# Kernel tuning notes

Measured on AMD Instinct MI355X. Metric: run time of the kernel, lower is better.

Reference implementation:

```python
import jax, jax.numpy as jnp
import numpy as np

N, D, E = 16384, 2048, 64   # tokens, d_model, num_experts
K = 9                        # self.k = min(k+1, num_experts) with k=8
EPS = 0.01
SIGMA = 1.0 / E              # Normal(0, 1/num_experts) stddev


def setup_inputs() -> dict:
    key = jax.random.key(0)
    ks = jax.random.split(key, 6)
    x = jax.random.normal(ks[0], (N, D), jnp.float32)
    Wr = jax.random.normal(ks[1], (D, E), jnp.float32) * 0.02
    br = jnp.zeros((E,), jnp.float32)
    Wn = jax.random.normal(ks[2], (D, E), jnp.float32) * 0.02
    bn = jnp.zeros((E,), jnp.float32)
    noise_eps = jax.random.normal(ks[3], (N, E), jnp.float32)
    # torch: (-empty.exponential_()).log() -> log of Exp(1) samples
    gumbel_noise = jnp.log(jax.random.exponential(ks[4], (N, E), jnp.float32))
    return {"x": x, "Wr": Wr, "br": br, "Wn": Wn, "bn": bn,
            "noise_eps": noise_eps, "gumbel_noise": gumbel_noise}


def reference(x, Wr, br, Wn, bn, noise_eps, gumbel_noise):
    raw_logits = x @ Wr + br                              # [N, E]
    noise_stddev = jax.nn.softplus(x @ Wn + bn) + EPS     # [N, E]
    noisy_logits = raw_logits + noise_eps * noise_stddev  # [N, E]

    top_vals, top_idx = jax.lax.top_k(noisy_logits, K)    # [N, K] sorted desc
    # scatter ones at top-k indices (indices unique per row)
    hard_mask = jax.nn.one_hot(top_idx, E, dtype=noisy_logits.dtype).sum(axis=1)  # [N, E]

    # gumbel-softmax straight-through relaxation
    mask_soft = jax.nn.softmax(noisy_logits + gumbel_noise, axis=-1)
    expert_mask = hard_mask - jax.lax.stop_gradient(mask_soft) + mask_soft

    route_prob = jax.nn.softmax(noisy_logits, axis=-1)    # [N, E]
    importance = jax.nn.softmax(raw_logits, axis=-1).sum(axis=0)  # [E]

    # load: P(raw + noise > threshold), Normal(0, 1/E) CDF per original
    threshold = top_vals[:, K - 1]                        # [N]
    z = (threshold[:, None] - raw_logits) / noise_stddev  # [N, E]
    cdf = 0.5 * (1.0 + jax.scipy.special.erf(z / (SIGMA * jnp.sqrt(jnp.float32(2.0)))))
    load = (1.0 - cdf).sum(axis=0)                        # [E]

    return (expert_mask, route_prob, importance, load)
```

## Files before the change

### kernel.cpp

```cpp
#include <hip/hip_runtime.h>
#include <hip/hip_bf16.h>
#include <math.h>

#define N_TOK 16384
#define DIM   2048
#define NE    64
#define TOPK  9

#define ROWS     32
#define DC       64
#define NCHUNK   (DIM / DC)
#define HALF     (NCHUNK / 2)
#define NTHREADS 512
#define NBUF     4

typedef short  short8  __attribute__((ext_vector_type(8)));
typedef float  float4_ __attribute__((ext_vector_type(4)));
typedef unsigned short ushort_t;

__device__ __forceinline__ void async16(const void* g, void* l) {
    __builtin_amdgcn_global_load_lds(
        (const __attribute__((address_space(1))) void*)g,
        (__attribute__((address_space(3))) void*)l, 16, 0, 0);
}

__device__ __forceinline__ unsigned pk2(float a, float b) {
    float2 f; f.x = a; f.y = b;
    __hip_bfloat162 h = __float22bfloat162_rn(f);
    unsigned u;
    __builtin_memcpy(&u, &h, 4);
    return u;
}

__device__ __forceinline__ void cvt8(const float4_ va, const float4_ vb,
                                     short8* h, short8* l) {
    union { short8 s; unsigned u[4]; } H, L;
    const float f[8] = {va[0], va[1], va[2], va[3], vb[0], vb[1], vb[2], vb[3]};
#pragma unroll
    for (int i = 0; i < 4; ++i) {
        const float a = f[2 * i], b = f[2 * i + 1];
        const unsigned p = pk2(a, b);
        H.u[i] = p;
        const float ha = __uint_as_float(p << 16);
        const float hb = __uint_as_float(p & 0xffff0000u);
        L.u[i] = pk2(a - ha, b - hb);
    }
    *h = H.s; *l = L.s;
}

__device__ __forceinline__ void wave_max64_2(float& a, float& b) {
#pragma unroll
    for (int off = 32; off > 0; off >>= 1) {
        const float ax = __shfl_xor(a, off, 64);
        const float bx = __shfl_xor(b, off, 64);
        a = fmaxf(a, ax);
        b = fmaxf(b, bx);
    }
}

__device__ __forceinline__ void wave_sum64_3(float& a, float& b, float& c) {
#pragma unroll
    for (int off = 32; off > 0; off >>= 1) {
        const float ax = __shfl_xor(a, off, 64);
        const float bx = __shfl_xor(b, off, 64);
        const float cx = __shfl_xor(c, off, 64);
        a += ax;
        b += bx;
        c += cx;
    }
}

__global__ __launch_bounds__(256)
void prep_w(const float* __restrict__ Wr, const float* __restrict__ Wn,
            ushort_t* __restrict__ wsW)
{
    const int gid = blockIdx.x * 256 + threadIdx.x;
    const int l   = gid & 63;
    const int ct  = (gid >> 6) & 7;
    const int kcg = gid >> 9;
    const int n   = ct * 16 + (l & 15);
    const int k0  = kcg * 32 + (l >> 4) * 8;
    const float* src = (n < NE) ? (Wr + n) : (Wn + (n - NE));
    union { short8 s; ushort_t us[8]; } H, L;
#pragma unroll
    for (int j = 0; j < 8; ++j) {
        const float v = src[(size_t)(k0 + j) * NE];
        const unsigned uv = __float_as_uint(v);
        const unsigned hb = (uv + 0x7fffu + ((uv >> 16) & 1u)) & 0xffff0000u;
        const float lo = v - __uint_as_float(hb);
        const unsigned ul = __float_as_uint(lo);
        H.us[j] = (ushort_t)(hb >> 16);
        L.us[j] = (ushort_t)((ul + 0x7fffu + ((ul >> 16) & 1u)) >> 16);
    }
    const size_t s0 = (size_t)(kcg * 8 + ct) * 2;
    *(short8*)(wsW + s0 * 512 + l * 8)         = H.s;
    *(short8*)(wsW + (s0 + 1) * 512 + l * 8)   = L.s;
}

struct BFrag { short8 h[2][2]; short8 l[2][2]; };

__device__ __forceinline__ void load_b(const char* __restrict__ wsB,
                                       int ch, int cg, int lane, BFrag& b) {
#pragma unroll
    for (int kc = 0; kc < 2; ++kc)
#pragma unroll
        for (int cc = 0; cc < 2; ++cc) {
            const size_t off = (size_t)(((ch * 2 + kc) * 8) + 2 * cg + cc) * 2048
                             + (size_t)lane * 16;
            b.h[kc][cc] = *(const short8*)(wsB + off);
            b.l[kc][cc] = *(const short8*)(wsB + off + 1024);
        }
}

__device__ __forceinline__ void mfma_chunk(const float* __restrict__ xb,
                                           const int (&aoff)[2][2],
                                           const BFrag& b,
                                           float4_ (&acc)[2][2]) {
#pragma unroll
    for (int kc = 0; kc < 2; ++kc)
#pragma unroll
        for (int rt = 0; rt < 2; ++rt) {
            const float4_ va = *(const float4_*)(xb + rt * 1024 + aoff[kc][0]);
            const float4_ vb = *(const float4_*)(xb + rt * 1024 + aoff[kc][1]);
            short8 ah, al;
            cvt8(va, vb, &ah, &al);
#pragma unroll
            for (int cc = 0; cc < 2; ++cc) {
                acc[rt][cc] = __builtin_amdgcn_mfma_f32_16x16x32_bf16(ah, b.h[kc][cc], acc[rt][cc], 0, 0, 0);
                acc[rt][cc] = __builtin_amdgcn_mfma_f32_16x16x32_bf16(al, b.h[kc][cc], acc[rt][cc], 0, 0, 0);
                acc[rt][cc] = __builtin_amdgcn_mfma_f32_16x16x32_bf16(ah, b.l[kc][cc], acc[rt][cc], 0, 0, 0);
            }
        }
}

__global__ __launch_bounds__(NTHREADS, 4)
void moe_main(const float* __restrict__ x,
              const float* __restrict__ br,
              const float* __restrict__ bn,
              const float* __restrict__ noise_eps,
              const float* __restrict__ gumbel,
              const ushort_t* __restrict__ wsW,
              float* __restrict__ out)
{
    __shared__ __align__(16) float smem[2 * NBUF * 2048];

    const int t    = threadIdx.x;
    const int lane = t & 63;
    const int w    = t >> 6;
    const int kh   = w >> 2;
    const int wv   = w & 3;
    const int c4   = lane & 15;
    const int q    = lane >> 4;
    const int row0 = blockIdx.x * ROWS;
    const int XB   = kh * (NBUF * 2048);

    const float* gxb[2];
    int lxo[2];
#pragma unroll
    for (int ii = 0; ii < 2; ++ii) {
        const int i  = 2 * wv + ii;
        const int r  = 4 * i + q;
        const int gk = c4 ^ (r & 15);
        gxb[ii] = x + (size_t)(row0 + r) * DIM + kh * (HALF * DC) + gk * 4;
        lxo[ii] = i * 256;
    }

    int aoff[2][2];
#pragma unroll
    for (int kc = 0; kc < 2; ++kc) {
        const int g0 = kc * 8 + q * 2;
        aoff[kc][0] = c4 * 64 + ((g0 ^ c4) * 4);
        aoff[kc][1] = c4 * 64 + (((g0 + 1) ^ c4) * 4);
    }

    float4_ acc[2][2];
#pragma unroll
    for (int rt = 0; rt < 2; ++rt)
#pragma unroll
        for (int cc = 0; cc < 2; ++cc)
            acc[rt][cc] = (float4_)(0.f);

    const char* wsB = (const char*)wsW;
    const int chb = kh * HALF;

#pragma unroll
    for (int p = 0; p < NBUF - 1; ++p)
#pragma unroll
        for (int ii = 0; ii < 2; ++ii)
            async16(gxb[ii] + p * DC, &smem[XB + p * 2048 + lxo[ii]]);

    BFrag bA, bB;
    load_b(wsB, chb, wv, lane, bA);

#pragma unroll 1
    for (int i = 0; i < HALF - 4; i += 2) {
        asm volatile("s_waitcnt vmcnt(12)" ::: "memory");
        __builtin_amdgcn_s_barrier();
        asm volatile("" ::: "memory");
        load_b(wsB, chb + i + 1, wv, lane, bB);
#pragma unroll
        for (int ii = 0; ii < 2; ++ii)
            async16(gxb[ii] + (i + 3) * DC, &smem[XB + ((i + 3) & 3) * 2048 + lxo[ii]]);
        __builtin_amdgcn_sched_barrier(0);
        mfma_chunk(&smem[XB + (i & 3) * 2048], aoff, bA, acc);

        asm volatile("s_waitcnt vmcnt(12)" ::: "memory");
        __builtin_amdgcn_s_barrier();
        asm volatile("" ::: "memory");
        load_b(wsB, chb + i + 2, wv, lane, bA);
#pragma unroll
        for (int ii = 0; ii < 2; ++ii)
            async16(gxb[ii] + (i + 4) * DC, &smem[XB + ((i + 4) & 3) * 2048 + lxo[ii]]);
        __builtin_amdgcn_sched_barrier(0);
        mfma_chunk(&smem[XB + ((i + 1) & 3) * 2048], aoff, bB, acc);
    }

    asm volatile("s_waitcnt vmcnt(12)" ::: "memory");
    __builtin_amdgcn_s_barrier();
    asm volatile("" ::: "memory");
    load_b(wsB, chb + 13, wv, lane, bB);
#pragma unroll
    for (int ii = 0; ii < 2; ++ii)
        async16(gxb[ii] + 15 * DC, &smem[XB + 3 * 2048 + lxo[ii]]);
    __builtin_amdgcn_sched_barrier(0);
    mfma_chunk(&smem[XB + 0 * 2048], aoff, bA, acc);

    asm volatile("s_waitcnt vmcnt(12)" ::: "memory");
    __builtin_amdgcn_s_barrier();
    asm volatile("" ::: "memory");
    load_b(wsB, chb + 14, wv, lane, bA);
    __builtin_amdgcn_sched_barrier(0);
    mfma_chunk(&smem[XB + 1 * 2048], aoff, bB, acc);

    asm volatile("s_waitcnt vmcnt(10)" ::: "memory");
    __builtin_amdgcn_s_barrier();
    asm volatile("" ::: "memory");
    load_b(wsB, chb + 15, wv, lane, bB);
    __builtin_amdgcn_sched_barrier(0);
    mfma_chunk(&smem[XB + 2 * 2048], aoff, bA, acc);

    asm volatile("s_waitcnt vmcnt(8)" ::: "memory");
    __builtin_amdgcn_s_barrier();
    asm volatile("" ::: "memory");
    __builtin_amdgcn_sched_barrier(0);
    mfma_chunk(&smem[XB + 3 * 2048], aoff, bB, acc);

    __syncthreads();
    {
        float* base = &smem[kh * 4160];
#pragma unroll
        for (int rt = 0; rt < 2; ++rt)
#pragma unroll
            for (int cc = 0; cc < 2; ++cc) {
                const int colg = (2 * wv + cc) * 16 + c4;
                float* bp = (colg < NE) ? base : (base + 2080);
                const int col = colg & 63;
#pragma unroll
                for (int v = 0; v < 4; ++v) {
                    const int row = rt * 16 + q * 4 + v;
                    bp[row * 65 + col] = acc[rt][cc][v];
                }
            }
    }
    __syncthreads();

    const float br_l = br[lane];
    const float bn_l = bn[lane];

    float epsv[4], gumv[4];
#pragma unroll
    for (int r = 0; r < 4; ++r) {
        const int row = row0 + w * 4 + r;
        epsv[r] = noise_eps[(size_t)row * NE + lane];
        gumv[r] = gumbel  [(size_t)row * NE + lane];
    }

    float imp_acc = 0.f, load_acc = 0.f;
    float* out_em   = out;
    float* out_rp   = out + (size_t)N_TOK * NE;
    float* out_imp  = out + (size_t)2 * N_TOK * NE;
    float* out_load = out_imp + NE;

#pragma unroll 1
    for (int r = 0; r < 4; ++r) {
        const int lrow = w * 4 + r;
        const int row  = row0 + lrow;
        const float raw = smem[lrow * 65 + lane] + smem[4160 + lrow * 65 + lane] + br_l;
        const float nl  = smem[2080 + lrow * 65 + lane] + smem[6240 + lrow * 65 + lane] + bn_l;
        const float sd = fmaxf(nl, 0.f) + log1pf(expf(-fabsf(nl))) + 0.01f;
        const float noisy = fmaf(epsv[r], sd, raw);

        const unsigned uk  = __float_as_uint(noisy);
        const unsigned key = uk ^ ((uk & 0x80000000u) ? 0xFFFFFFFFu : 0x80000000u);
        unsigned res = 0;
#pragma unroll
        for (int bit = 31; bit >= 0; --bit) {
            const unsigned cand = res | (1u << bit);
            const int cnt = __popcll(__ballot(key >= cand));
            if (cnt >= TOPK) res = cand;
        }
        const float thr  = __uint_as_float(res ^ ((res & 0x80000000u) ? 0x80000000u : 0xFFFFFFFFu));
        const float hard = (key >= res) ? 1.f : 0.f;

        const float g = noisy + gumv[r];
        float mg = g, mr = raw;
        wave_max64_2(mg, mr);

        const float eg = expf(g - mg);
        const float en = expf(noisy - thr);
        const float er = expf(raw - mr);
        float sg = eg, sn = en, sr = er;
        wave_sum64_3(sg, sn, sr);

        const float ms = eg / sg;
        const float em = (hard - ms) + ms;
        const float rp = en / sn;
        imp_acc += er / sr;

        const float z = (thr - raw) / sd;
        load_acc += 0.5f * erfcf(z * 45.254833995939045f);

        out_em[(size_t)row * NE + lane] = em;
        out_rp[(size_t)row * NE + lane] = rp;
    }

    __syncthreads();
    smem[w * 64 + lane]       = imp_acc;
    smem[512 + w * 64 + lane] = load_acc;
    __syncthreads();
    if (w == 0) {
        float s1 = 0.f, s2 = 0.f;
#pragma unroll
        for (int i = 0; i < 8; ++i) {
            s1 += smem[i * 64 + lane];
            s2 += smem[512 + i * 64 + lane];
        }
        atomicAdd(&out_imp[lane], s1);
        atomicAdd(&out_load[lane], s2);
    }
}

extern "C" void kernel_launch(void* const* d_in, const int* in_sizes, int n_in,
                              void* d_out, int out_size, void* d_ws, size_t ws_size,
                              hipStream_t stream)
{
    const float* x         = (const float*)d_in[0];
    const float* Wr        = (const float*)d_in[1];
    const float* br        = (const float*)d_in[2];
    const float* Wn        = (const float*)d_in[3];
    const float* bn        = (const float*)d_in[4];
    const float* noise_eps = (const float*)d_in[5];
    const float* gumbel    = (const float*)d_in[6];
    float* out = (float*)d_out;
    ushort_t* wsW = (ushort_t*)d_ws;

    (void)hipMemsetAsync((char*)d_out + (size_t)2 * N_TOK * NE * sizeof(float), 0,
                         2 * NE * sizeof(float), stream);
    prep_w<<<128, 256, 0, stream>>>(Wr, Wn, wsW);
    moe_main<<<N_TOK / ROWS, NTHREADS, 0, stream>>>(
        x, br, bn, noise_eps, gumbel, wsW, out);
}
```

Measured before the change: 246.6 us.

## Drop split-K halves; use 16-row blocks with 256 threads over full K

```diff
diff --git a/kernel.cpp b/kernel.cpp
--- a/kernel.cpp
+++ b/kernel.cpp
@@ -7,11 +7,10 @@
 #define NE    64
 #define TOPK  9
 
-#define ROWS     32
+#define ROWS     16
 #define DC       64
 #define NCHUNK   (DIM / DC)
-#define HALF     (NCHUNK / 2)
-#define NTHREADS 512
+#define NTHREADS 256
 #define NBUF     4
 
 typedef short  short8  __attribute__((ext_vector_type(8)));
@@ -100,12 +99,12 @@
 struct BFrag { short8 h[2][2]; short8 l[2][2]; };
 
 __device__ __forceinline__ void load_b(const char* __restrict__ wsB,
-                                       int ch, int cg, int lane, BFrag& b) {
+                                       int ch, int w, int lane, BFrag& b) {
 #pragma unroll
     for (int kc = 0; kc < 2; ++kc)
 #pragma unroll
         for (int cc = 0; cc < 2; ++cc) {
-            const size_t off = (size_t)(((ch * 2 + kc) * 8) + 2 * cg + cc) * 2048
+            const size_t off = (size_t)(((ch * 2 + kc) * 8) + 2 * w + cc) * 2048
                              + (size_t)lane * 16;
             b.h[kc][cc] = *(const short8*)(wsB + off);
             b.l[kc][cc] = *(const short8*)(wsB + off + 1024);
@@ -115,22 +114,20 @@
 __device__ __forceinline__ void mfma_chunk(const float* __restrict__ xb,
                                            const int (&aoff)[2][2],
                                            const BFrag& b,
-                                           float4_ (&acc)[2][2]) {
-#pragma unroll
-    for (int kc = 0; kc < 2; ++kc)
-#pragma unroll
-        for (int rt = 0; rt < 2; ++rt) {
-            const float4_ va = *(const float4_*)(xb + rt * 1024 + aoff[kc][0]);
-            const float4_ vb = *(const float4_*)(xb + rt * 1024 + aoff[kc][1]);
-            short8 ah, al;
-            cvt8(va, vb, &ah, &al);
-#pragma unroll
-            for (int cc = 0; cc < 2; ++cc) {
-                acc[rt][cc] = __builtin_amdgcn_mfma_f32_16x16x32_bf16(ah, b.h[kc][cc], acc[rt][cc], 0, 0, 0);
-                acc[rt][cc] = __builtin_amdgcn_mfma_f32_16x16x32_bf16(al, b.h[kc][cc], acc[rt][cc], 0, 0, 0);
-                acc[rt][cc] = __builtin_amdgcn_mfma_f32_16x16x32_bf16(ah, b.l[kc][cc], acc[rt][cc], 0, 0, 0);
-            }
+                                           float4_ (&acc)[2]) {
+#pragma unroll
+    for (int kc = 0; kc < 2; ++kc) {
+        const float4_ va = *(const float4_*)(xb + aoff[kc][0]);
+        const float4_ vb = *(const float4_*)(xb + aoff[kc][1]);
+        short8 ah, al;
+        cvt8(va, vb, &ah, &al);
+#pragma unroll
+        for (int cc = 0; cc < 2; ++cc) {
+            acc[cc] = __builtin_amdgcn_mfma_f32_16x16x32_bf16(ah, b.h[kc][cc], acc[cc], 0, 0, 0);
+            acc[cc] = __builtin_amdgcn_mfma_f32_16x16x32_bf16(al, b.h[kc][cc], acc[cc], 0, 0, 0);
+            acc[cc] = __builtin_amdgcn_mfma_f32_16x16x32_bf16(ah, b.l[kc][cc], acc[cc], 0, 0, 0);
         }
+    }
 }
 
 __global__ __launch_bounds__(NTHREADS, 4)
@@ -142,28 +139,19 @@
               const ushort_t* __restrict__ wsW,
               float* __restrict__ out)
 {
-    __shared__ __align__(16) float smem[2 * NBUF * 2048];
+    __shared__ __align__(16) float smem[4352];
 
     const int t    = threadIdx.x;
     const int lane = t & 63;
     const int w    = t >> 6;
-    const int kh   = w >> 2;
-    const int wv   = w & 3;
     const int c4   = lane & 15;
     const int q    = lane >> 4;
     const int row0 = blockIdx.x * ROWS;
-    const int XB   = kh * (NBUF * 2048);
-
-    const float* gxb[2];
-    int lxo[2];
-#pragma unroll
-    for (int ii = 0; ii < 2; ++ii) {
-        const int i  = 2 * wv + ii;
-        const int r  = 4 * i + q;
-        const int gk = c4 ^ (r & 15);
-        gxb[ii] = x + (size_t)(row0 + r) * DIM + kh * (HALF * DC) + gk * 4;
-        lxo[ii] = i * 256;
-    }
+
+    const int  srow = 4 * w + q;
+    const int  sgk  = c4 ^ (srow & 15);
+    const float* gxb = x + (size_t)(row0 + srow) * DIM + sgk * 4;
+    const int  lxo  = w * 256;
 
     int aoff[2][2];
 #pragma unroll
@@ -173,99 +161,65 @@
         aoff[kc][1] = c4 * 64 + (((g0 + 1) ^ c4) * 4);
     }
 
-    float4_ acc[2][2];
-#pragma unroll
-    for (int rt = 0; rt < 2; ++rt)
-#pragma unroll
-        for (int cc = 0; cc < 2; ++cc)
-            acc[rt][cc] = (float4_)(0.f);
+    float4_ acc[2];
+    acc[0] = (float4_)(0.f);
+    acc[1] = (float4_)(0.f);
 
     const char* wsB = (const char*)wsW;
-    const int chb = kh * HALF;
 
 #pragma unroll
     for (int p = 0; p < NBUF - 1; ++p)
-#pragma unroll
-        for (int ii = 0; ii < 2; ++ii)
-            async16(gxb[ii] + p * DC, &smem[XB + p * 2048 + lxo[ii]]);
+        async16(gxb + p * DC, &smem[p * 1024 + lxo]);
 
     BFrag bA, bB;
-    load_b(wsB, chb, wv, lane, bA);
+    load_b(wsB, 0, w, lane, bA);
 
 #pragma unroll 1
-    for (int i = 0; i < HALF - 4; i += 2) {
-        asm volatile("s_waitcnt vmcnt(12)" ::: "memory");
+    for (int i = 0; i < NCHUNK - 4; i += 2) {
+        asm volatile("s_waitcnt vmcnt(10)" ::: "memory");
         __builtin_amdgcn_s_barrier();
         asm volatile("" ::: "memory");
-        load_b(wsB, chb + i + 1, wv, lane, bB);
-#pragma unroll
-        for (int ii = 0; ii < 2; ++ii)
-            async16(gxb[ii] + (i + 3) * DC, &smem[XB + ((i + 3) & 3) * 2048 + lxo[ii]]);
+        load_b(wsB, i + 1, w, lane, bB);
+        async16(gxb + (i + 3) * DC, &smem[((i + 3) & 3) * 1024 + lxo]);
         __builtin_amdgcn_sched_barrier(0);
-        mfma_chunk(&smem[XB + (i & 3) * 2048], aoff, bA, acc);
-
-        asm volatile("s_waitcnt vmcnt(12)" ::: "memory");
+        mfma_chunk(&smem[(i & 3) * 1024], aoff, bA, acc);
+
+        asm volatile("s_waitcnt vmcnt(10)" ::: "memory");
         __builtin_amdgcn_s_barrier();
         asm volatile("" ::: "memory");
-        load_b(wsB, chb + i + 2, wv, lane, bA);
-#pragma unroll
-        for (int ii = 0; ii < 2; ++ii)
-            async16(gxb[ii] + (i + 4) * DC, &smem[XB + ((i + 4) & 3) * 2048 + lxo[ii]]);
+        load_b(wsB, i + 2, w, lane, bA);
+        async16(gxb + (i + 4) * DC, &smem[((i + 4) & 3) * 1024 + lxo]);
         __builtin_amdgcn_sched_barrier(0);
-        mfma_chunk(&smem[XB + ((i + 1) & 3) * 2048], aoff, bB, acc);
-    }
-
-    asm volatile("s_waitcnt vmcnt(12)" ::: "memory");
-    __builtin_amdgcn_s_barrier();
-    asm volatile("" ::: "memory");
-    load_b(wsB, chb + 13, wv, lane, bB);
-#pragma unroll
-    for (int ii = 0; ii < 2; ++ii)
-        async16(gxb[ii] + 15 * DC, &smem[XB + 3 * 2048 + lxo[ii]]);
-    __builtin_amdgcn_sched_barrier(0);
-    mfma_chunk(&smem[XB + 0 * 2048], aoff, bA, acc);
-
-    asm volatile("s_waitcnt vmcnt(12)" ::: "memory");
-    __builtin_amdgcn_s_barrier();
-    asm volatile("" ::: "memory");
-    load_b(wsB, chb + 14, wv, lane, bA);
-    __builtin_amdgcn_sched_barrier(0);
-    mfma_chunk(&smem[XB + 1 * 2048], aoff, bB, acc);
+        mfma_chunk(&smem[((i + 1) & 3) * 1024], aoff, bB, acc);
+    }
 
     asm volatile("s_waitcnt vmcnt(10)" ::: "memory");
     __builtin_amdgcn_s_barrier();
     asm volatile("" ::: "memory");
-    load_b(wsB, chb + 15, wv, lane, bB);
+    load_b(wsB, 29, w, lane, bB);
+    async16(gxb + 31 * DC, &smem[3 * 1024 + lxo]);
     __builtin_amdgcn_sched_barrier(0);
-    mfma_chunk(&smem[XB + 2 * 2048], aoff, bA, acc);
+    mfma_chunk(&smem[0 * 1024], aoff, bA, acc);
+
+    asm volatile("s_waitcnt vmcnt(10)" ::: "memory");
+    __builtin_amdgcn_s_barrier();
+    asm volatile("" ::: "memory");
+    load_b(wsB, 30, w, lane, bA);
+    __builtin_amdgcn_sched_barrier(0);
+    mfma_chunk(&smem[1 * 1024], aoff, bB, acc);
+
+    asm volatile("s_waitcnt vmcnt(9)" ::: "memory");
+    __builtin_amdgcn_s_barrier();
+    asm volatile("" ::: "memory");
+    load_b(wsB, 31, w, lane, bB);
+    __builtin_amdgcn_sched_barrier(0);
+    mfma_chunk(&smem[2 * 1024], aoff, bA, acc);
 
     asm volatile("s_waitcnt vmcnt(8)" ::: "memory");
     __builtin_amdgcn_s_barrier();
     asm volatile("" ::: "memory");
     __builtin_amdgcn_sched_barrier(0);
-    mfma_chunk(&smem[XB + 3 * 2048], aoff, bB, acc);
-
-    __syncthreads();
-    {
-        float* base = &smem[kh * 4160];
-#pragma unroll
-        for (int rt = 0; rt < 2; ++rt)
-#pragma unroll
-            for (int cc = 0; cc < 2; ++cc) {
-                const int colg = (2 * wv + cc) * 16 + c4;
-                float* bp = (colg < NE) ? base : (base + 2080);
-                const int col = colg & 63;
-#pragma unroll
-                for (int v = 0; v < 4; ++v) {
-                    const int row = rt * 16 + q * 4 + v;
-                    bp[row * 65 + col] = acc[rt][cc][v];
-                }
-            }
-    }
-    __syncthreads();
-
-    const float br_l = br[lane];
-    const float bn_l = bn[lane];
+    mfma_chunk(&smem[3 * 1024], aoff, bB, acc);
 
     float epsv[4], gumv[4];
 #pragma unroll
@@ -274,6 +228,25 @@
         epsv[r] = noise_eps[(size_t)row * NE + lane];
         gumv[r] = gumbel  [(size_t)row * NE + lane];
     }
+
+    __syncthreads();
+    float* rawS = &smem[0];
+    float* noiS = &smem[2080];
+#pragma unroll
+    for (int cc = 0; cc < 2; ++cc) {
+        const int colg = (2 * w + cc) * 16 + c4;
+        float* basep = (colg < NE) ? rawS : noiS;
+        const int col = colg & 63;
+#pragma unroll
+        for (int v = 0; v < 4; ++v) {
+            const int row = q * 4 + v;
+            basep[row * 65 + col] = acc[cc][v];
+        }
+    }
+    __syncthreads();
+
+    const float br_l = br[lane];
+    const float bn_l = bn[lane];
 
     float imp_acc = 0.f, load_acc = 0.f;
     float* out_em   = out;
@@ -285,8 +258,8 @@
     for (int r = 0; r < 4; ++r) {
         const int lrow = w * 4 + r;
         const int row  = row0 + lrow;
-        const float raw = smem[lrow * 65 + lane] + smem[4160 + lrow * 65 + lane] + br_l;
-        const float nl  = smem[2080 + lrow * 65 + lane] + smem[6240 + lrow * 65 + lane] + bn_l;
+        const float raw = rawS[lrow * 65 + lane] + br_l;
+        const float nl  = noiS[lrow * 65 + lane] + bn_l;
         const float sd = fmaxf(nl, 0.f) + log1pf(expf(-fabsf(nl))) + 0.01f;
         const float noisy = fmaf(epsv[r], sd, raw);
 
@@ -326,15 +299,11 @@
 
     __syncthreads();
     smem[w * 64 + lane]       = imp_acc;
-    smem[512 + w * 64 + lane] = load_acc;
+    smem[256 + w * 64 + lane] = load_acc;
     __syncthreads();
     if (w == 0) {
-        float s1 = 0.f, s2 = 0.f;
-#pragma unroll
-        for (int i = 0; i < 8; ++i) {
-            s1 += smem[i * 64 + lane];
-            s2 += smem[512 + i * 64 + lane];
-        }
+        const float s1 = smem[lane] + smem[64 + lane] + smem[128 + lane] + smem[192 + lane];
+        const float s2 = smem[256 + lane] + smem[320 + lane] + smem[384 + lane] + smem[448 + lane];
         atomicAdd(&out_imp[lane], s1);
         atomicAdd(&out_load[lane], s2);
     }
```

Measured after the change: 261.2 us. +5.9%, slower.
